# Kernel tuning notes

Hardware: AMD Instinct MI355X
Metric: run time of the kernel (lower is better)

## Reference

```python
import jax, jax.numpy as jnp
import numpy as np
from math import sqrt

B, L, S = 8, 1024, 1000
D_MODEL, D_LLM, H, E = 1024, 4096, 16, 64  # d_keys = d_model // n_heads = 64


def setup_inputs() -> dict:
    key = jax.random.key(0)
    ks = jax.random.split(key, 11)
    s = 0.02
    return {
        "target_embedding": jax.random.normal(ks[0], (B, L, D_MODEL), jnp.float32),
        "source_embedding": jax.random.normal(ks[1], (S, D_LLM), jnp.float32),
        "value_embedding": jax.random.normal(ks[2], (S, D_LLM), jnp.float32),
        "Wq": jax.random.normal(ks[3], (D_MODEL, H * E), jnp.float32) * s,
        "bq": jnp.zeros((H * E,), jnp.float32),
        "Wk": jax.random.normal(ks[4], (D_LLM, H * E), jnp.float32) * s,
        "bk": jnp.zeros((H * E,), jnp.float32),
        "Wv": jax.random.normal(ks[5], (D_LLM, H * E), jnp.float32) * s,
        "bv": jnp.zeros((H * E,), jnp.float32),
        "Wo": jax.random.normal(ks[6], (H * E, D_LLM), jnp.float32) * s,
        "bo": jnp.zeros((D_LLM,), jnp.float32),
    }


def reference(target_embedding, source_embedding, value_embedding,
              Wq, bq, Wk, bk, Wv, bv, Wo, bo):
    b, l, _ = target_embedding.shape
    # projections
    q = (target_embedding @ Wq + bq).reshape(b, l, H, E)          # (B,L,H,E)
    k = (source_embedding @ Wk + bk).reshape(-1, H, E)            # (S,H,E) shared across batch
    v = (value_embedding @ Wv + bv).reshape(-1, H, E)             # (S,H,E)
    scale = 1.0 / sqrt(E)
    scores = jnp.einsum('blhe,she->bhls', q, k) * scale           # (B,H,L,S)
    A = jax.nn.softmax(scores, axis=-1)                           # dropout is identity (eval)
    out = jnp.einsum('bhls,she->blhe', A, v).reshape(b, l, H * E)
    return out @ Wo + bo                                          # (B,L,d_llm)
```

## Files before the change

kernel.cpp:

```cpp
#include <hip/hip_runtime.h>
#include <hip/hip_bf16.h>
#include <math.h>

#define B_SZ 8
#define L_SZ 1024
#define S_SZ 1000
#define DM   1024
#define DL   4096
#define NH   16
#define EH   64
#define QK_SCALE 0.180336880f
#define NTILES 32

typedef __bf16 bf16x8 __attribute__((ext_vector_type(8)));
typedef __bf16 bf16x4 __attribute__((ext_vector_type(4)));
typedef float  f32x4  __attribute__((ext_vector_type(4)));

__device__ __forceinline__ void async16(const void* g, void* l) {
    __builtin_amdgcn_global_load_lds(
        (const __attribute__((address_space(1))) void*)g,
        (__attribute__((address_space(3))) void*)l, 16, 0, 0);
}

__global__ __launch_bounds__(256) void prep_kernel(
    const float* __restrict__ target, const float* __restrict__ source,
    const float* __restrict__ value,
    const float* __restrict__ Wq, const float* __restrict__ Wk,
    const float* __restrict__ Wv, const float* __restrict__ Wo,
    __bf16* __restrict__ Tb, __bf16* __restrict__ Sb, __bf16* __restrict__ Vb,
    __bf16* __restrict__ WqT, __bf16* __restrict__ WkT,
    __bf16* __restrict__ WvT, __bf16* __restrict__ WoT)
{
    __shared__ float t[64][68];
    int bid = blockIdx.x;
    if (bid < 16192) {
        const float* in; __bf16* out; int i;
        if (bid < 8192)       { in = target; out = Tb; i = bid * 256 + threadIdx.x; }
        else if (bid < 12192) { in = source; out = Sb; i = (bid - 8192)  * 256 + threadIdx.x; }
        else                  { in = value;  out = Vb; i = (bid - 12192) * 256 + threadIdx.x; }
        float4 x = ((const float4*)in)[i];
        bf16x4 y;
        y.x = (__bf16)x.x; y.y = (__bf16)x.y;
        y.z = (__bf16)x.z; y.w = (__bf16)x.w;
        ((bf16x4*)out)[i] = y;
        return;
    }
    bid -= 16192;
    const float* W; __bf16* WT; int K, N, bx, by;
    if (bid < 256)       { W = Wq; WT = WqT; K = DM; N = DM; int u = bid;        bx = u & 15; by = u >> 4; }
    else if (bid < 1280) { W = Wk; WT = WkT; K = DL; N = DM; int u = bid - 256;  bx = u & 15; by = u >> 4; }
    else if (bid < 2304) { W = Wv; WT = WvT; K = DL; N = DM; int u = bid - 1280; bx = u & 15; by = u >> 4; }
    else                 { W = Wo; WT = WoT; K = DM; N = DL; int u = bid - 2304; bx = u & 63; by = u >> 6; }
    const int k0 = by * 64, n0 = bx * 64;
    const int tx = threadIdx.x & 15, ty = threadIdx.x >> 4;

#pragma unroll
    for (int tt = 0; tt < 4; ++tt) {
        int r = ty + 16 * tt;
        float4 x = *(const float4*)&W[(size_t)(k0 + r) * N + n0 + 4 * tx];
        *(float4*)&t[r][4 * tx] = x;
    }
    __syncthreads();
#pragma unroll
    for (int tt = 0; tt < 4; ++tt) {
        int n = ty + 16 * tt;
        bf16x4 y;
        y.x = (__bf16)t[4 * tx + 0][n];
        y.y = (__bf16)t[4 * tx + 1][n];
        y.z = (__bf16)t[4 * tx + 2][n];
        y.w = (__bf16)t[4 * tx + 3][n];
        *(bf16x4*)&WT[(size_t)(n0 + n) * K + k0 + 4 * tx] = y;
    }
}

__device__ __forceinline__ void pipe_body(
    const __bf16* __restrict__ A, const __bf16* __restrict__ BT, int ld,
    const float* __restrict__ bias, void* __restrict__ Cv, int ldc,
    int M, int m0, int n0, float oscale, int omode,
    __bf16 (*sA)[256 * 32], __bf16 (*sB)[256 * 32])
{
    const int tid  = threadIdx.x;
    const int lane = tid & 63, wave = tid >> 6;
    const int wr = wave >> 2, wc = wave & 3;
    const int lm = lane & 15, lq = lane >> 4;

    f32x4 acc[8][4];
#pragma unroll
    for (int i = 0; i < 8; ++i)
#pragma unroll
        for (int j = 0; j < 4; ++j)
            acc[i][j] = (f32x4){0.f, 0.f, 0.f, 0.f};

    auto stage = [&](int slot, int t) {
        const int k0 = t * 32;
#pragma unroll
        for (int i = 0; i < 2; ++i) {
            int cc = i * 512 + tid;
            int r  = cc >> 2;
            int sg = (cc & 3) ^ ((r >> 1) & 3);
            int gm = m0 + r; if (gm >= M) gm = M - 1;
            async16(A  + (size_t)gm * ld + k0 + sg * 8,
                    (char*)sA[slot] + cc * 16);
            async16(BT + (size_t)(n0 + r) * ld + k0 + sg * 8,
                    (char*)sB[slot] + cc * 16);
        }
    };

    bf16x8 fa0[8], fb0[4], fa1[8], fb1[4];

    auto read_frags = [&](int slot, bf16x8 (&fa)[8], bf16x8 (&fb)[4]) {
#pragma unroll
        for (int ni = 0; ni < 4; ++ni) {
            int rr = wc * 64 + ni * 16 + lm;
            fb[ni] = *(const bf16x8*)((const char*)sB[slot]
                     + rr * 64 + ((lq ^ ((rr >> 1) & 3)) * 16));
        }
#pragma unroll
        for (int mi = 0; mi < 8; ++mi) {
            int rr = wr * 128 + mi * 16 + lm;
            fa[mi] = *(const bf16x8*)((const char*)sA[slot]
                     + rr * 64 + ((lq ^ ((rr >> 1) & 3)) * 16));
        }
    };

    auto mfma_all = [&](bf16x8 (&fa)[8], bf16x8 (&fb)[4]) {
        __builtin_amdgcn_s_setprio(1);
#pragma unroll
        for (int mi = 0; mi < 8; ++mi)
#pragma unroll
            for (int ni = 0; ni < 4; ++ni)
                acc[mi][ni] = __builtin_amdgcn_mfma_f32_16x16x32_bf16(
                    fa[mi], fb[ni], acc[mi][ni], 0, 0, 0);
        __builtin_amdgcn_s_setprio(0);
    };

    stage(0, 0); stage(1, 1); stage(2, 2);
    asm volatile("s_waitcnt vmcnt(4)" ::: "memory");
    __builtin_amdgcn_s_barrier();
    __builtin_amdgcn_sched_barrier(0);
    read_frags(0, fa0, fb0);

    for (int tt = 0; tt < NTILES; tt += 2) {
        if (tt + 3 < NTILES) stage((tt + 3) & 3, tt + 3);
        read_frags((tt + 1) & 3, fa1, fb1);
        mfma_all(fa0, fb0);
        if (tt + 3 < NTILES)
            asm volatile("s_waitcnt vmcnt(4)" ::: "memory");
        else
            asm volatile("s_waitcnt vmcnt(0)" ::: "memory");
        asm volatile("s_waitcnt lgkmcnt(0)" ::: "memory");
        __builtin_amdgcn_sched_barrier(0);
        __builtin_amdgcn_s_barrier();
        __builtin_amdgcn_sched_barrier(0);

        if (tt + 4 < NTILES) stage((tt + 4) & 3, tt + 4);
        if (tt + 2 < NTILES) read_frags((tt + 2) & 3, fa0, fb0);
        mfma_all(fa1, fb1);
        if (tt + 2 < NTILES) {
            if (tt + 4 < NTILES)
                asm volatile("s_waitcnt vmcnt(4)" ::: "memory");
            else
                asm volatile("s_waitcnt vmcnt(0)" ::: "memory");
            asm volatile("s_waitcnt lgkmcnt(0)" ::: "memory");
            __builtin_amdgcn_sched_barrier(0);
            __builtin_amdgcn_s_barrier();
            __builtin_amdgcn_sched_barrier(0);
        }
    }

#pragma unroll
    for (int mi = 0; mi < 8; ++mi) {
        int gm0 = m0 + wr * 128 + mi * 16 + lq * 4;
#pragma unroll
        for (int ni = 0; ni < 4; ++ni) {
            int gn = n0 + wc * 64 + ni * 16 + lm;
            float bv = (omode == 2) ? 0.f : bias[gn];
#pragma unroll
            for (int r = 0; r < 4; ++r) {
                int gm = gm0 + r;
                if (gm < M) {
                    float val = acc[mi][ni][r] + bv;
                    if (omode == 0)
                        ((__bf16*)Cv)[(size_t)gm * ldc + gn] = (__bf16)(val * oscale);
                    else
                        ((float*)Cv)[(size_t)gm * ldc + gn] = val;
                }
            }
        }
    }
}

__global__ __launch_bounds__(512, 2) void qkv_pipe_kernel(
    const __bf16* __restrict__ Tb, const __bf16* __restrict__ Sb,
    const __bf16* __restrict__ Vb,
    const __bf16* __restrict__ WqT, const __bf16* __restrict__ WkT,
    const __bf16* __restrict__ WvT,
    const float* __restrict__ bq,
    __bf16* __restrict__ qb, float* __restrict__ kpart, float* __restrict__ vpart)
{
    __shared__ __bf16 sA[4][256 * 32];
    __shared__ __bf16 sB[4][256 * 32];
    int bid = blockIdx.x;
    const __bf16 *A, *BT; const float* bias; void* Cv;
    int ld, M, m0, n0, omode; float osc;
    if (bid < 128) {
        A = Tb; BT = WqT; bias = bq; Cv = qb; ld = DM; M = B_SZ * L_SZ;
        m0 = (bid >> 2) * 256; n0 = (bid & 3) * 256; omode = 0; osc = QK_SCALE;
    } else if (bid < 192) {
        int u = bid - 128, ks = u >> 4, v = u & 15;
        A = Sb + ks * 1024; BT = WkT + ks * 1024; bias = nullptr;
        Cv = kpart + (size_t)ks * 1024000; ld = DL; M = S_SZ;
        m0 = (v >> 2) * 256; n0 = (v & 3) * 256; omode = 2; osc = 1.f;
    } else {
        int u = bid - 192, ks = u >> 4, v = u & 15;
        A = Vb + ks * 1024; BT = WvT + ks * 1024; bias = nullptr;
        Cv = vpart + (size_t)ks * 1024000; ld = DL; M = S_SZ;
        m0 = (v >> 2) * 256; n0 = (v & 3) * 256; omode = 2; osc = 1.f;
    }
    pipe_body(A, BT, ld, bias, Cv, DM, M, m0, n0, osc, omode, sA, sB);
}

__global__ __launch_bounds__(512, 2) void gemm_o_pipe_kernel(
    const __bf16* __restrict__ ab, const __bf16* __restrict__ WoT,
    const float* __restrict__ bo, float* __restrict__ out)
{
    __shared__ __bf16 sA[4][256 * 32];
    __shared__ __bf16 sB[4][256 * 32];
    int bid = blockIdx.x;
    bid = (bid & 7) * 64 + (bid >> 3);
    pipe_body(ab, WoT, DM, bo, out, DL, B_SZ * L_SZ,
              (bid >> 4) * 256, (bid & 15) * 256, 1.f, 1, sA, sB);
}

__global__ __launch_bounds__(256) void combine_kv_kernel(
    const float* __restrict__ kpart, const float* __restrict__ vpart,
    const float* __restrict__ bk, const float* __restrict__ bv,
    __bf16* __restrict__ kb, __bf16* __restrict__ vtb)
{
    __shared__ float t[64][68];
    const int bid = blockIdx.x, tid = threadIdx.x;
    if (bid < 1000) {
        int e4 = bid * 256 + tid;
        int col = (e4 & 255) * 4;
        float4 s = *(const float4*)&bk[col];
#pragma unroll
        for (int j = 0; j < 4; ++j) {
            float4 pp = *(const float4*)&kpart[(size_t)j * 1024000 + (size_t)e4 * 4];
            s.x += pp.x; s.y += pp.y; s.z += pp.z; s.w += pp.w;
        }
        bf16x4 y;
        y.x = (__bf16)s.x; y.y = (__bf16)s.y;
        y.z = (__bf16)s.z; y.w = (__bf16)s.w;
        ((bf16x4*)kb)[e4] = y;
    } else {
        int u = bid - 1000;
        int d0 = (u & 15) * 64, s0 = (u >> 4) * 64;
#pragma unroll
        for (int tt = 0; tt < 4; ++tt) {
            int idx = tt * 256 + tid;
            int r = idx >> 4, c4 = idx & 15;
            float4 s = {0.f, 0.f, 0.f, 0.f};
            if (s0 + r < S_SZ) {
                s = *(const float4*)&bv[d0 + c4 * 4];
#pragma unroll
                for (int j = 0; j < 4; ++j) {
                    float4 pp = *(const float4*)&vpart[(size_t)j * 1024000
                                + (size_t)(s0 + r) * 1024 + d0 + c4 * 4];
                    s.x += pp.x; s.y += pp.y; s.z += pp.z; s.w += pp.w;
                }
            }
            *(float4*)&t[r][c4 * 4] = s;
        }
        __syncthreads();
#pragma unroll
        for (int tt = 0; tt < 2; ++tt) {
            int idx = tt * 256 + tid;
            int d = idx >> 3, ch = idx & 7;
            bf16x8 o;
#pragma unroll
            for (int j = 0; j < 8; ++j) o[j] = (__bf16)t[ch * 8 + j][d];
            *(bf16x8*)&vtb[(size_t)(d0 + d) * 1024 + s0 + ch * 8] = o;
        }
    }
}

__global__ __launch_bounds__(256) void attn_mfma_kernel(
    const __bf16* __restrict__ q,
    const __bf16* __restrict__ k,
    const __bf16* __restrict__ vt,
    __bf16* __restrict__ o)
{
    __shared__ __bf16 Ks [2][64 * 64];
    __shared__ __bf16 Vts[2][64 * 64];
    __shared__ __bf16 Ps [4][32 * 72];

    const int tid  = threadIdx.x;
    const int lane = tid & 63;
    const int wave = tid >> 6;
    const int lm   = lane & 15;
    const int lq   = lane >> 4;
    const int bh = blockIdx.y;
    const int b  = bh >> 4;
    const int h  = bh & 15;
    const int l0 = blockIdx.x * 128;
    const int row0 = b * L_SZ + l0 + wave * 32;

    bf16x8 qf[2][2];
#pragma unroll
    for (int mt = 0; mt < 2; ++mt)
#pragma unroll
        for (int ks = 0; ks < 2; ++ks)
            qf[mt][ks] = *(const bf16x8*)&q[(size_t)(row0 + mt * 16 + lm) * DM
                                           + h * 64 + ks * 32 + lq * 8];

    f32x4 oa[2][4];
    f32x4 lacc[2];
    float m_run[2][4];
#pragma unroll
    for (int mt = 0; mt < 2; ++mt) {
        lacc[mt] = (f32x4){0.f, 0.f, 0.f, 0.f};
#pragma unroll
        for (int r = 0; r < 4; ++r) m_run[mt][r] = -1e30f;
#pragma unroll
        for (int et = 0; et < 4; ++et) oa[mt][et] = (f32x4){0.f, 0.f, 0.f, 0.f};
    }

    bf16x8 vones;
#pragma unroll
    for (int j = 0; j < 8; ++j) vones[j] = (__bf16)1.0f;

    auto stage = [&](int bi, int s0v) {
#pragma unroll
        for (int t = 0; t < 2; ++t) {
            int cc = t * 256 + tid;
            int r = cc >> 3, segL = cc & 7;
            int segG = segL ^ (r & 7);
            int sg = s0v + r; if (sg >= S_SZ) sg = S_SZ - 1;
            async16(k  + (size_t)sg * DM + h * 64 + segG * 8,
                    (char*)Ks[bi] + cc * 16);
            async16(vt + (size_t)(h * 64 + r) * 1024 + s0v + segG * 8,
                    (char*)Vts[bi] + cc * 16);
        }
    };

    stage(0, 0);
    int cur = 0;

    for (int s0 = 0; s0 < S_SZ; s0 += 64) {
        __syncthreads();
        if (s0 + 64 < S_SZ) stage(cur ^ 1, s0 + 64);

        f32x4 sc[2][4];
#pragma unroll
        for (int mt = 0; mt < 2; ++mt)
#pragma unroll
            for (int nt = 0; nt < 4; ++nt)
                sc[mt][nt] = (f32x4){0.f, 0.f, 0.f, 0.f};
#pragma unroll
        for (int ks = 0; ks < 2; ++ks)
#pragma unroll
            for (int nt = 0; nt < 4; ++nt) {
                bf16x8 bK = *(const bf16x8*)((const char*)Ks[cur]
                    + (nt * 16 + lm) * 128 + (((ks * 4 + lq) ^ (lm & 7)) * 16));
#pragma unroll
                for (int mt = 0; mt < 2; ++mt)
                    sc[mt][nt] = __builtin_amdgcn_mfma_f32_16x16x32_bf16(
                        qf[mt][ks], bK, sc[mt][nt], 0, 0, 0);
            }

        if (s0 + 64 > S_SZ) {
#pragma unroll
            for (int nt = 0; nt < 4; ++nt) {
                bool masked = (s0 + nt * 16 + lm >= S_SZ);
                if (masked)
#pragma unroll
                    for (int mt = 0; mt < 2; ++mt)
#pragma unroll
                        for (int r = 0; r < 4; ++r) sc[mt][nt][r] = -1e30f;
            }
        }

        float pm[2][4];
        bool ok = true;
#pragma unroll
        for (int mt = 0; mt < 2; ++mt)
#pragma unroll
            for (int r = 0; r < 4; ++r) {
                pm[mt][r] = fmaxf(fmaxf(sc[mt][0][r], sc[mt][1][r]),
                                  fmaxf(sc[mt][2][r], sc[mt][3][r]));
                ok = ok && (pm[mt][r] <= m_run[mt][r] + 8.f);
            }
        if (!__all((int)ok)) {
#pragma unroll
            for (int mt = 0; mt < 2; ++mt)
#pragma unroll
                for (int r = 0; r < 4; ++r) {
                    float mx = pm[mt][r];
#pragma unroll
                    for (int off = 1; off < 16; off <<= 1)
                        mx = fmaxf(mx, __shfl_xor(mx, off));
                    float mnew  = fmaxf(m_run[mt][r], mx);
                    float alpha = __builtin_amdgcn_exp2f(m_run[mt][r] - mnew);
                    m_run[mt][r] = mnew;
                    lacc[mt][r] *= alpha;
#pragma unroll
                    for (int et = 0; et < 4; ++et)
                        oa[mt][et][r] *= alpha;
                }
        }

#pragma unroll
        for (int mt = 0; mt < 2; ++mt)
#pragma unroll
            for (int r = 0; r < 4; ++r) {
                int prow = (mt * 16 + lq * 4 + r) * 72;
#pragma unroll
                for (int nt = 0; nt < 4; ++nt) {
                    float pv = __builtin_amdgcn_exp2f(sc[mt][nt][r] - m_run[mt][r]);
                    Ps[wave][prow + nt * 16 + lm] = (__bf16)pv;
                }
            }

        asm volatile("s_waitcnt lgkmcnt(0)" ::: "memory");

#pragma unroll
        for (int ks = 0; ks < 2; ++ks) {
            bf16x8 aP[2];
#pragma unroll
            for (int mt = 0; mt < 2; ++mt)
                aP[mt] = *(const bf16x8*)&Ps[wave][(mt * 16 + lm) * 72
                                                  + ks * 32 + lq * 8];
#pragma unroll
            for (int mt = 0; mt < 2; ++mt)
                lacc[mt] = __builtin_amdgcn_mfma_f32_16x16x32_bf16(
                    aP[mt], vones, lacc[mt], 0, 0, 0);
#pragma unroll
            for (int et = 0; et < 4; ++et) {
                bf16x8 bV = *(const bf16x8*)((const char*)Vts[cur]
                    + (et * 16 + lm) * 128 + (((ks * 4 + lq) ^ (lm & 7)) * 16));
#pragma unroll
                for (int mt = 0; mt < 2; ++mt)
                    oa[mt][et] = __builtin_amdgcn_mfma_f32_16x16x32_bf16(
                        aP[mt], bV, oa[mt][et], 0, 0, 0);
            }
        }
        cur ^= 1;
    }

#pragma unroll
    for (int mt = 0; mt < 2; ++mt)
#pragma unroll
        for (int r = 0; r < 4; ++r) {
            float inv = 1.f / lacc[mt][r];
            size_t rowi = (size_t)(row0 + mt * 16 + lq * 4 + r) * DM + h * 64;
#pragma unroll
            for (int et = 0; et < 4; ++et)
                o[rowi + et * 16 + lm] = (__bf16)(oa[mt][et][r] * inv);
        }
}

extern "C" void kernel_launch(void* const* d_in, const int* in_sizes, int n_in,
                              void* d_out, int out_size, void* d_ws, size_t ws_size,
                              hipStream_t stream)
{
    const float* target = (const float*)d_in[0];
    const float* source = (const float*)d_in[1];
    const float* value  = (const float*)d_in[2];
    const float* Wq = (const float*)d_in[3];
    const float* bq = (const float*)d_in[4];
    const float* Wk = (const float*)d_in[5];
    const float* bk = (const float*)d_in[6];
    const float* Wv = (const float*)d_in[7];
    const float* bv = (const float*)d_in[8];
    const float* Wo = (const float*)d_in[9];
    const float* bo = (const float*)d_in[10];
    float* out = (float*)d_out;

    char* p = (char*)d_ws;
    __bf16* Tb  = (__bf16*)(p);
    __bf16* Sb  = (__bf16*)(p + 16777216);
    __bf16* vtb = (__bf16*)(p + 16777216);
    __bf16* kb  = (__bf16*)(p + 24969216);
    __bf16* WqT = (__bf16*)(p + 29065216);
    __bf16* WoT = (__bf16*)(p + 31162368);
    char*   R   =           p + 39550976;
    __bf16* Vb  = (__bf16*)(R);
    __bf16* WvT = (__bf16*)(R + 8192000);
    __bf16* WkT = (__bf16*)(R + 16580608);
    __bf16* qb    = (__bf16*)d_out;
    float*  kpart = (float*)((char*)d_out + 16777216);
    float*  vpart = (float*)((char*)d_out + 33161216);
    __bf16* ab    = (__bf16*)(p);

    prep_kernel<<<19520, 256, 0, stream>>>(target, source, value, Wq, Wk, Wv, Wo,
                                           Tb, Sb, Vb, WqT, WkT, WvT, WoT);
    qkv_pipe_kernel<<<256, 512, 0, stream>>>(Tb, Sb, Vb, WqT, WkT, WvT,
                                             bq, qb, kpart, vpart);
    combine_kv_kernel<<<1256, 256, 0, stream>>>(kpart, vpart, bk, bv, kb, vtb);
    attn_mfma_kernel<<<dim3(8, 128), 256, 0, stream>>>(qb, kb, vtb, ab);
    gemm_o_pipe_kernel<<<512, 512, 0, stream>>>(ab, WoT, bo, out);
}
```

Before: 459.5 us.

## Split GEMM pipeline stages into halves interleaving loads, LDS reads and MFMAs

Restructures the software-pipelined GEMM main loop so each k-tile's global-to-LDS staging, fragment reads and MFMA block are split into two halves. Half the A fragments are computed while the other half is read, with an extra workgroup barrier between halves. This aims to spread memory issue across the MFMA stream and hide LDS latency better. It adds barriers and a more intricate waitcnt schedule, which raises the risk of sync overhead or ordering mistakes.

```diff
diff --git a/kernel.cpp b/kernel.cpp
--- a/kernel.cpp
+++ b/kernel.cpp
@@ -91,73 +91,105 @@
         for (int j = 0; j < 4; ++j)
             acc[i][j] = (f32x4){0.f, 0.f, 0.f, 0.f};
 
-    auto stage = [&](int slot, int t) {
+    auto stage_half = [&](int slot, int t, int h) {
         const int k0 = t * 32;
-#pragma unroll
-        for (int i = 0; i < 2; ++i) {
-            int cc = i * 512 + tid;
-            int r  = cc >> 2;
-            int sg = (cc & 3) ^ ((r >> 1) & 3);
-            int gm = m0 + r; if (gm >= M) gm = M - 1;
-            async16(A  + (size_t)gm * ld + k0 + sg * 8,
-                    (char*)sA[slot] + cc * 16);
-            async16(BT + (size_t)(n0 + r) * ld + k0 + sg * 8,
-                    (char*)sB[slot] + cc * 16);
-        }
+        int cc = h * 512 + tid;
+        int r  = cc >> 2;
+        int sg = (cc & 3) ^ ((r >> 1) & 3);
+        int gm = m0 + r; if (gm >= M) gm = M - 1;
+        async16(A  + (size_t)gm * ld + k0 + sg * 8, (char*)sA[slot] + cc * 16);
+        async16(BT + (size_t)(n0 + r) * ld + k0 + sg * 8, (char*)sB[slot] + cc * 16);
     };
 
     bf16x8 fa0[8], fb0[4], fa1[8], fb1[4];
 
-    auto read_frags = [&](int slot, bf16x8 (&fa)[8], bf16x8 (&fb)[4]) {
+    auto read_fb = [&](int slot, bf16x8 (&fb)[4]) {
 #pragma unroll
         for (int ni = 0; ni < 4; ++ni) {
             int rr = wc * 64 + ni * 16 + lm;
             fb[ni] = *(const bf16x8*)((const char*)sB[slot]
                      + rr * 64 + ((lq ^ ((rr >> 1) & 3)) * 16));
         }
-#pragma unroll
-        for (int mi = 0; mi < 8; ++mi) {
+    };
+    auto read_fa_lo = [&](int slot, bf16x8 (&fa)[8]) {
+#pragma unroll
+        for (int mi = 0; mi < 4; ++mi) {
             int rr = wr * 128 + mi * 16 + lm;
             fa[mi] = *(const bf16x8*)((const char*)sA[slot]
                      + rr * 64 + ((lq ^ ((rr >> 1) & 3)) * 16));
         }
     };
-
-    auto mfma_all = [&](bf16x8 (&fa)[8], bf16x8 (&fb)[4]) {
+    auto read_fa_hi = [&](int slot, bf16x8 (&fa)[8]) {
+#pragma unroll
+        for (int mi = 4; mi < 8; ++mi) {
+            int rr = wr * 128 + mi * 16 + lm;
+            fa[mi] = *(const bf16x8*)((const char*)sA[slot]
+                     + rr * 64 + ((lq ^ ((rr >> 1) & 3)) * 16));
+        }
+    };
+    auto mfma_lo = [&](bf16x8 (&fa)[8], bf16x8 (&fb)[4]) {
         __builtin_amdgcn_s_setprio(1);
 #pragma unroll
-        for (int mi = 0; mi < 8; ++mi)
+        for (int mi = 0; mi < 4; ++mi)
 #pragma unroll
             for (int ni = 0; ni < 4; ++ni)
                 acc[mi][ni] = __builtin_amdgcn_mfma_f32_16x16x32_bf16(
                     fa[mi], fb[ni], acc[mi][ni], 0, 0, 0);
         __builtin_amdgcn_s_setprio(0);
     };
-
-    stage(0, 0); stage(1, 1); stage(2, 2);
-    asm volatile("s_waitcnt vmcnt(4)" ::: "memory");
+    auto mfma_hi = [&](bf16x8 (&fa)[8], bf16x8 (&fb)[4]) {
+        __builtin_amdgcn_s_setprio(1);
+#pragma unroll
+        for (int mi = 4; mi < 8; ++mi)
+#pragma unroll
+            for (int ni = 0; ni < 4; ++ni)
+                acc[mi][ni] = __builtin_amdgcn_mfma_f32_16x16x32_bf16(
+                    fa[mi], fb[ni], acc[mi][ni], 0, 0, 0);
+        __builtin_amdgcn_s_setprio(0);
+    };
+
+    stage_half(0, 0, 0); stage_half(0, 0, 1);
+    stage_half(1, 1, 0); stage_half(1, 1, 1);
+    stage_half(2, 2, 0); stage_half(2, 2, 1);
+    asm volatile("s_waitcnt vmcnt(8)" ::: "memory");
+    __builtin_amdgcn_sched_barrier(0);
     __builtin_amdgcn_s_barrier();
     __builtin_amdgcn_sched_barrier(0);
-    read_frags(0, fa0, fb0);
+    read_fb(0, fb0); read_fa_lo(0, fa0); read_fa_hi(0, fa0);
+    asm volatile("s_waitcnt vmcnt(4)" ::: "memory");
+    asm volatile("s_waitcnt lgkmcnt(0)" ::: "memory");
+    __builtin_amdgcn_sched_barrier(0);
+    __builtin_amdgcn_s_barrier();
+    __builtin_amdgcn_sched_barrier(0);
 
     for (int tt = 0; tt < NTILES; tt += 2) {
-        if (tt + 3 < NTILES) stage((tt + 3) & 3, tt + 3);
-        read_frags((tt + 1) & 3, fa1, fb1);
-        mfma_all(fa0, fb0);
-        if (tt + 3 < NTILES)
-            asm volatile("s_waitcnt vmcnt(4)" ::: "memory");
-        else
-            asm volatile("s_waitcnt vmcnt(0)" ::: "memory");
-        asm volatile("s_waitcnt lgkmcnt(0)" ::: "memory");
-        __builtin_amdgcn_sched_barrier(0);
+        if (tt + 3 < NTILES) stage_half((tt + 3) & 3, tt + 3, 0);
+        if (tt + 1 < NTILES) { read_fb((tt + 1) & 3, fb1); read_fa_lo((tt + 1) & 3, fa1); }
+        mfma_lo(fa0, fb0);
         __builtin_amdgcn_s_barrier();
-        __builtin_amdgcn_sched_barrier(0);
-
-        if (tt + 4 < NTILES) stage((tt + 4) & 3, tt + 4);
-        if (tt + 2 < NTILES) read_frags((tt + 2) & 3, fa0, fb0);
-        mfma_all(fa1, fb1);
-        if (tt + 2 < NTILES) {
-            if (tt + 4 < NTILES)
+        if (tt + 3 < NTILES) stage_half((tt + 3) & 3, tt + 3, 1);
+        if (tt + 1 < NTILES) read_fa_hi((tt + 1) & 3, fa1);
+        mfma_hi(fa0, fb0);
+        if (tt + 1 < NTILES) {
+            if (tt + 3 < NTILES)
+                asm volatile("s_waitcnt vmcnt(4)" ::: "memory");
+            else
+                asm volatile("s_waitcnt vmcnt(0)" ::: "memory");
+            asm volatile("s_waitcnt lgkmcnt(0)" ::: "memory");
+            __builtin_amdgcn_sched_barrier(0);
+            __builtin_amdgcn_s_barrier();
+            __builtin_amdgcn_sched_barrier(0);
+        }
+        const int t1 = tt + 1;
+        if (t1 + 3 < NTILES) stage_half((t1 + 3) & 3, t1 + 3, 0);
+        if (t1 + 1 < NTILES) { read_fb((t1 + 1) & 3, fb0); read_fa_lo((t1 + 1) & 3, fa0); }
+        mfma_lo(fa1, fb1);
+        __builtin_amdgcn_s_barrier();
+        if (t1 + 3 < NTILES) stage_half((t1 + 3) & 3, t1 + 3, 1);
+        if (t1 + 1 < NTILES) read_fa_hi((t1 + 1) & 3, fa0);
+        mfma_hi(fa1, fb1);
+        if (t1 + 1 < NTILES) {
+            if (t1 + 3 < NTILES)
                 asm volatile("s_waitcnt vmcnt(4)" ::: "memory");
             else
                 asm volatile("s_waitcnt vmcnt(0)" ::: "memory");
```

After: 458.8 us. No clear change (-0.1%).

## Restructure GEMM pipeline into 64-wide K tiles with four-phase interleaved staging

Applied to the files above, without the earlier changes.

Changes the shared GEMM mainloop from a 4-slot ring of 32-wide K tiles to a double-buffered scheme of 64-wide K tiles, each split into two 32-wide halves. Each iteration now runs four phases in which A-fragment reads, MFMA batches over half the M rows, and async global-to-LDS loads of A and B halves are interleaved, with barriers between phases. The LDS swizzle also changes from (r>>1)&3 to r&3. The aim is to keep fewer A fragments live in registers and to overlap loads with MFMA more finely, in exchange for many more barriers per K step.

```diff
diff --git a/kernel.cpp b/kernel.cpp
--- a/kernel.cpp
+++ b/kernel.cpp
@@ -10,7 +10,7 @@
 #define NH   16
 #define EH   64
 #define QK_SCALE 0.180336880f
-#define NTILES 32
+#define NT64 16
 
 typedef __bf16 bf16x8 __attribute__((ext_vector_type(8)));
 typedef __bf16 bf16x4 __attribute__((ext_vector_type(4)));
@@ -77,7 +77,7 @@
     const __bf16* __restrict__ A, const __bf16* __restrict__ BT, int ld,
     const float* __restrict__ bias, void* __restrict__ Cv, int ldc,
     int M, int m0, int n0, float oscale, int omode,
-    __bf16 (*sA)[256 * 32], __bf16 (*sB)[256 * 32])
+    __bf16* sAb, __bf16* sBb)
 {
     const int tid  = threadIdx.x;
     const int lane = tid & 63, wave = tid >> 6;
@@ -91,82 +91,100 @@
         for (int j = 0; j < 4; ++j)
             acc[i][j] = (f32x4){0.f, 0.f, 0.f, 0.f};
 
-    auto stage = [&](int slot, int t) {
-        const int k0 = t * 32;
+    auto stageA = [&](int buf, int kk, int t) {
+        const int k0 = t * 64 + kk * 32;
+        char* base = (char*)sAb + (buf * 2 + kk) * 16384;
 #pragma unroll
         for (int i = 0; i < 2; ++i) {
             int cc = i * 512 + tid;
-            int r  = cc >> 2;
-            int sg = (cc & 3) ^ ((r >> 1) & 3);
+            int r = cc >> 2;
+            int sg = (cc & 3) ^ (r & 3);
             int gm = m0 + r; if (gm >= M) gm = M - 1;
-            async16(A  + (size_t)gm * ld + k0 + sg * 8,
-                    (char*)sA[slot] + cc * 16);
-            async16(BT + (size_t)(n0 + r) * ld + k0 + sg * 8,
-                    (char*)sB[slot] + cc * 16);
+            async16(A + (size_t)gm * ld + k0 + sg * 8, base + cc * 16);
         }
     };
-
-    bf16x8 fa0[8], fb0[4], fa1[8], fb1[4];
-
-    auto read_frags = [&](int slot, bf16x8 (&fa)[8], bf16x8 (&fb)[4]) {
+    auto stageB = [&](int buf, int kk, int t) {
+        const int k0 = t * 64 + kk * 32;
+        char* base = (char*)sBb + (buf * 2 + kk) * 16384;
+#pragma unroll
+        for (int i = 0; i < 2; ++i) {
+            int cc = i * 512 + tid;
+            int r = cc >> 2;
+            int sg = (cc & 3) ^ (r & 3);
+            async16(BT + (size_t)(n0 + r) * ld + k0 + sg * 8, base + cc * 16);
+        }
+    };
+
+    bf16x8 fbk0[4], fbk1[4], fa[4];
+    auto read_fb = [&](int buf, int kk, bf16x8 (&fb)[4]) {
+        const char* base = (const char*)sBb + (buf * 2 + kk) * 16384;
 #pragma unroll
         for (int ni = 0; ni < 4; ++ni) {
-            int rr = wc * 64 + ni * 16 + lm;
-            fb[ni] = *(const bf16x8*)((const char*)sB[slot]
-                     + rr * 64 + ((lq ^ ((rr >> 1) & 3)) * 16));
-        }
-#pragma unroll
-        for (int mi = 0; mi < 8; ++mi) {
-            int rr = wr * 128 + mi * 16 + lm;
-            fa[mi] = *(const bf16x8*)((const char*)sA[slot]
-                     + rr * 64 + ((lq ^ ((rr >> 1) & 3)) * 16));
+            int r = wc * 64 + ni * 16 + lm;
+            fb[ni] = *(const bf16x8*)(base + r * 64 + ((lq ^ (r & 3)) * 16));
         }
     };
-
-    auto mfma_all = [&](bf16x8 (&fa)[8], bf16x8 (&fb)[4]) {
+    auto read_fa = [&](int buf, int kk, int mo) {
+        const char* base = (const char*)sAb + (buf * 2 + kk) * 16384;
+#pragma unroll
+        for (int i = 0; i < 4; ++i) {
+            int r = wr * 128 + (mo + i) * 16 + lm;
+            fa[i] = *(const bf16x8*)(base + r * 64 + ((lq ^ (r & 3)) * 16));
+        }
+    };
+    auto mfma16 = [&](bf16x8 (&fb)[4], int mo) {
         __builtin_amdgcn_s_setprio(1);
 #pragma unroll
-        for (int mi = 0; mi < 8; ++mi)
+        for (int i = 0; i < 4; ++i)
 #pragma unroll
             for (int ni = 0; ni < 4; ++ni)
-                acc[mi][ni] = __builtin_amdgcn_mfma_f32_16x16x32_bf16(
-                    fa[mi], fb[ni], acc[mi][ni], 0, 0, 0);
+                acc[mo + i][ni] = __builtin_amdgcn_mfma_f32_16x16x32_bf16(
+                    fa[i], fb[ni], acc[mo + i][ni], 0, 0, 0);
         __builtin_amdgcn_s_setprio(0);
     };
 
-    stage(0, 0); stage(1, 1); stage(2, 2);
+#define PHASE_SYNC() do { \
+        __builtin_amdgcn_s_barrier(); \
+        asm volatile("s_waitcnt lgkmcnt(0)" ::: "memory"); \
+        __builtin_amdgcn_sched_barrier(0); } while (0)
+
+    stageA(0, 0, 0); stageB(0, 0, 0); stageA(0, 1, 0); stageB(0, 1, 0);
+    stageA(1, 0, 1); stageB(1, 0, 1);
     asm volatile("s_waitcnt vmcnt(4)" ::: "memory");
+    __builtin_amdgcn_sched_barrier(0);
     __builtin_amdgcn_s_barrier();
-    __builtin_amdgcn_sched_barrier(0);
-    read_frags(0, fa0, fb0);
-
-    for (int tt = 0; tt < NTILES; tt += 2) {
-        if (tt + 3 < NTILES) stage((tt + 3) & 3, tt + 3);
-        read_frags((tt + 1) & 3, fa1, fb1);
-        mfma_all(fa0, fb0);
-        if (tt + 3 < NTILES)
+
+    for (int t = 0; t < NT64; ++t) {
+        const int b = t & 1, bn = b ^ 1;
+        if (t + 1 < NT64) stageA(bn, 1, t + 1);
+        read_fb(b, 0, fbk0);
+        read_fa(b, 0, 0);
+        PHASE_SYNC();
+        mfma16(fbk0, 0);
+        __builtin_amdgcn_s_barrier();
+        if (t + 1 < NT64) stageB(bn, 1, t + 1);
+        read_fa(b, 0, 4);
+        PHASE_SYNC();
+        mfma16(fbk0, 4);
+        __builtin_amdgcn_s_barrier();
+        if (t + 2 < NT64) stageA(b, 0, t + 2);
+        read_fb(b, 1, fbk1);
+        read_fa(b, 1, 0);
+        PHASE_SYNC();
+        mfma16(fbk1, 0);
+        __builtin_amdgcn_s_barrier();
+        if (t + 2 < NT64) stageB(b, 0, t + 2);
+        read_fa(b, 1, 4);
+        PHASE_SYNC();
+        mfma16(fbk1, 4);
+        if (t + 2 < NT64)
             asm volatile("s_waitcnt vmcnt(4)" ::: "memory");
         else
             asm volatile("s_waitcnt vmcnt(0)" ::: "memory");
-        asm volatile("s_waitcnt lgkmcnt(0)" ::: "memory");
         __builtin_amdgcn_sched_barrier(0);
         __builtin_amdgcn_s_barrier();
-        __builtin_amdgcn_sched_barrier(0);
-
-        if (tt + 4 < NTILES) stage((tt + 4) & 3, tt + 4);
-        if (tt + 2 < NTILES) read_frags((tt + 2) & 3, fa0, fb0);
-        mfma_all(fa1, fb1);
-        if (tt + 2 < NTILES) {
-            if (tt + 4 < NTILES)
-                asm volatile("s_waitcnt vmcnt(4)" ::: "memory");
-            else
-                asm volatile("s_waitcnt vmcnt(0)" ::: "memory");
-            asm volatile("s_waitcnt lgkmcnt(0)" ::: "memory");
-            __builtin_amdgcn_sched_barrier(0);
-            __builtin_amdgcn_s_barrier();
-            __builtin_amdgcn_sched_barrier(0);
-        }
-    }
+    }
+#undef PHASE_SYNC
 
 #pragma unroll
     for (int mi = 0; mi < 8; ++mi) {
@@ -198,8 +216,8 @@
     const float* __restrict__ bq,
     __bf16* __restrict__ qb, float* __restrict__ kpart, float* __restrict__ vpart)
 {
-    __shared__ __bf16 sA[4][256 * 32];
-    __shared__ __bf16 sB[4][256 * 32];
+    __shared__ __bf16 sA[2][2][256 * 32];
+    __shared__ __bf16 sB[2][2][256 * 32];
     int bid = blockIdx.x;
     const __bf16 *A, *BT; const float* bias; void* Cv;
     int ld, M, m0, n0, omode; float osc;
@@ -217,19 +235,21 @@
         Cv = vpart + (size_t)ks * 1024000; ld = DL; M = S_SZ;
         m0 = (v >> 2) * 256; n0 = (v & 3) * 256; omode = 2; osc = 1.f;
     }
-    pipe_body(A, BT, ld, bias, Cv, DM, M, m0, n0, osc, omode, sA, sB);
+    pipe_body(A, BT, ld, bias, Cv, DM, M, m0, n0, osc, omode,
+              &sA[0][0][0], &sB[0][0][0]);
 }
 
 __global__ __launch_bounds__(512, 2) void gemm_o_pipe_kernel(
     const __bf16* __restrict__ ab, const __bf16* __restrict__ WoT,
     const float* __restrict__ bo, float* __restrict__ out)
 {
-    __shared__ __bf16 sA[4][256 * 32];
-    __shared__ __bf16 sB[4][256 * 32];
+    __shared__ __bf16 sA[2][2][256 * 32];
+    __shared__ __bf16 sB[2][2][256 * 32];
     int bid = blockIdx.x;
     bid = (bid & 7) * 64 + (bid >> 3);
     pipe_body(ab, WoT, DM, bo, out, DL, B_SZ * L_SZ,
-              (bid >> 4) * 256, (bid & 15) * 256, 1.f, 1, sA, sB);
+              (bid >> 4) * 256, (bid & 15) * 256, 1.f, 1,
+              &sA[0][0][0], &sB[0][0][0]);
 }
 
 __global__ __launch_bounds__(256) void combine_kv_kernel(
```

Result: faster. 444.7 us (-3.2%).
